# Performance work log

Hardware: AMD Instinct MI355X
Metric: run time of the kernel (lower is better)

## Reference

```python
import jax, jax.numpy as jnp
import numpy as np

B, N, DIM = 2, 2048, 1024
HEADS, DIM_HEAD = 16, 64
INNER = HEADS * DIM_HEAD  # 1024
SCALE = DIM_HEAD ** -0.5


def setup_inputs() -> dict:
    key = jax.random.key(0)
    ks = jax.random.split(key, 6)
    s = lambda k, shape, fan: jax.random.normal(k, shape, jnp.float32) * (fan ** -0.5)
    return {
        "x": jax.random.normal(ks[0], (B, N, DIM), jnp.float32),
        "similarity": jax.random.normal(ks[1], (B, N), jnp.float32),
        "Wq": s(ks[2], (DIM, INNER), DIM),
        "Wkv": s(ks[3], (DIM, 2 * INNER), DIM),
        "Wo": s(ks[4], (INNER, DIM), INNER),
        "bo": jnp.zeros((DIM,), jnp.float32),
    }


def reference(x, similarity, Wq, Wkv, Wo, bo):
    b, n, _ = x.shape
    h, d = HEADS, DIM_HEAD
    # projections (context = x, self-attention)
    q = (x @ Wq).reshape(b, n, h, d).transpose(0, 2, 1, 3)        # b h n d
    kv = x @ Wkv                                                   # b n 2*inner
    k, v = jnp.split(kv, 2, axis=-1)
    k = k.reshape(b, n, h, d).transpose(0, 2, 1, 3)
    v = v.reshape(b, n, h, d).transpose(0, 2, 1, 3)
    dots = jnp.einsum('bhid,bhjd->bhij', q, k) * SCALE             # b h n n
    # similarity [b,n] -> broadcast as per-query row bias [b,1,n,1]
    dots = dots + similarity[:, None, :, None]
    attn = jax.nn.softmax(dots, axis=-1)
    out = jnp.einsum('bhij,bhjd->bhid', attn, v)                   # b h n d
    out = out.transpose(0, 2, 1, 3).reshape(b, n, h * d)           # b n inner
    return out @ Wo + bo
```

## Files before the change

### kernel.cpp

```cpp
#include <hip/hip_runtime.h>


typedef __attribute__((ext_vector_type(8))) short short8;
typedef __attribute__((ext_vector_type(4))) float float4_;
typedef __attribute__((ext_vector_type(4))) unsigned short ushort4_;

#define MFMA(a, b, c) __builtin_amdgcn_mfma_f32_16x16x32_bf16((a), (b), (c), 0, 0, 0)

static __device__ __forceinline__ unsigned short f2bf(float f) {
    union { float f; unsigned int u; } v; v.f = f;
    unsigned int r = v.u + 0x7FFFu + ((v.u >> 16) & 1u);
    return (unsigned short)(r >> 16);
}

static __device__ __forceinline__ void gld16(const void* g, void* l) {
    __builtin_amdgcn_global_load_lds(
        (__attribute__((address_space(1))) void*)(g),
        (__attribute__((address_space(3))) void*)(l), 16, 0, 0);
}

__global__ __launch_bounds__(256) void prep(
    const float* __restrict__ X, const float* __restrict__ Wq,
    const float* __restrict__ Wkv, const float* __restrict__ Wo,
    unsigned short* __restrict__ xb, unsigned short* __restrict__ Wt,
    unsigned short* __restrict__ Wot)
{
    const int bid = blockIdx.x, t = threadIdx.x;
    if (bid >= 1024) {
        const int b = bid - 1024;
        const float4_* src = (const float4_*)X;
        ushort4_* dst = (ushort4_*)xb;
        #pragma unroll
        for (int g = 0; g < 8; ++g) {
            const int idx = b * 2048 + g * 256 + t;
            float4_ v = src[idx];
            ushort4_ o;
            o[0] = f2bf(v[0]); o[1] = f2bf(v[1]);
            o[2] = f2bf(v[2]); o[3] = f2bf(v[3]);
            dst[idx] = o;
        }
        return;
    }
    __shared__ float tile[64][65];
    const float* src; unsigned short* dst; int N, kt, nt, drow0;
    if (bid < 256)      { src = Wq;  N = 1024; kt = bid & 15;       nt = bid >> 4;       dst = Wt;  drow0 = nt * 64; }
    else if (bid < 768) { src = Wkv; N = 2048; kt = (bid-256) & 15; nt = (bid-256) >> 4; dst = Wt;  drow0 = 1024 + nt * 64; }
    else                { src = Wo;  N = 1024; kt = (bid-768) & 15; nt = (bid-768) >> 4; dst = Wot; drow0 = nt * 64; }
    const int k0 = kt * 64, n0 = nt * 64;
    const int r0 = t >> 6, c = t & 63;
    #pragma unroll
    for (int i = 0; i < 16; ++i) {
        const int r = i * 4 + r0;
        tile[r][c] = src[(size_t)(k0 + r) * N + n0 + c];
    }
    __syncthreads();
    #pragma unroll
    for (int i = 0; i < 16; ++i) {
        const int rn = i * 4 + r0;
        dst[(size_t)(drow0 + rn) * 1024 + k0 + c] = f2bf(tile[c][rn]);
    }
}

__global__ __launch_bounds__(256) void qkv_gemm2(
    const unsigned short* __restrict__ xb, const unsigned short* __restrict__ Wt,
    unsigned short* __restrict__ q_ws, unsigned short* __restrict__ k_ws,
    unsigned short* __restrict__ vt_ws)
{
    __shared__ unsigned short As[128 * 64];
    __shared__ unsigned short Bs[128 * 64];
    const int t = threadIdx.x, wave = t >> 6, lane = t & 63;
    const int L = lane & 15, quad = lane >> 4;
    const int mb = blockIdx.x / 24, nb = blockIdx.x % 24;
    const int m0 = mb * 128, n0 = nb * 128;
    const int wr = wave >> 1, wc = wave & 1;

    float4_ z = {0.f, 0.f, 0.f, 0.f};
    float4_ acc[4][4];
    #pragma unroll
    for (int i = 0; i < 4; ++i)
        #pragma unroll
        for (int j = 0; j < 4; ++j) acc[i][j] = z;

    const unsigned short* gA[4]; const unsigned short* gB[4];
    unsigned short* lA[4]; unsigned short* lB[4];
    #pragma unroll
    for (int j = 0; j < 4; ++j) {
        const int cid = wave * 256 + j * 64 + lane;
        const int row = cid >> 3, pc = cid & 7;
        const int lch = pc ^ (row & 7);
        gA[j] = xb + (size_t)(m0 + row) * 1024 + lch * 8;
        gB[j] = Wt + (size_t)(n0 + row) * 1024 + lch * 8;
        lA[j] = As + wave * 2048 + j * 512;
        lB[j] = Bs + wave * 2048 + j * 512;
    }

    for (int kc = 0; kc < 1024; kc += 64) {
        #pragma unroll
        for (int j = 0; j < 4; ++j) {
            gld16(gA[j] + kc, lA[j]);
            gld16(gB[j] + kc, lB[j]);
        }
        __syncthreads();
        #pragma unroll
        for (int ks = 0; ks < 2; ++ks) {
            short8 af[4], bfr[4];
            #pragma unroll
            for (int mt = 0; mt < 4; ++mt) {
                const int rl = wr * 64 + mt * 16 + L;
                af[mt] = *(const short8*)(As + rl * 64 + (((ks * 4 + quad) ^ (L & 7)) << 3));
            }
            #pragma unroll
            for (int nt = 0; nt < 4; ++nt) {
                const int rl = wc * 64 + nt * 16 + L;
                bfr[nt] = *(const short8*)(Bs + rl * 64 + (((ks * 4 + quad) ^ (L & 7)) << 3));
            }
            #pragma unroll
            for (int mt = 0; mt < 4; ++mt)
                #pragma unroll
                for (int nt = 0; nt < 4; ++nt)
                    acc[mt][nt] = MFMA(af[mt], bfr[nt], acc[mt][nt]);
        }
        __syncthreads();
    }

    const int b = m0 >> 11;
    const int type = n0 >> 10;
    #pragma unroll
    for (int mt = 0; mt < 4; ++mt) {
        const int m = (m0 & 2047) + wr * 64 + mt * 16 + quad * 4;
        #pragma unroll
        for (int nt = 0; nt < 4; ++nt) {
            const int cl = (n0 & 1023) + wc * 64 + nt * 16 + L;
            const int h = cl >> 6, d = cl & 63;
            float4_ v = acc[mt][nt];
            if (type == 0) {
                unsigned short* p = q_ws + ((size_t)(b * 16 + h) * 2048 + m) * 64 + d;
                #pragma unroll
                for (int r = 0; r < 4; ++r) p[(size_t)r * 64] = f2bf(v[r] * 0.18033688011f);
            } else if (type == 1) {
                unsigned short* p = k_ws + ((size_t)(b * 16 + h) * 2048 + m) * 64 + d;
                #pragma unroll
                for (int r = 0; r < 4; ++r) p[(size_t)r * 64] = f2bf(v[r]);
            } else {
                ushort4_ pk;
                pk[0] = f2bf(v[0]); pk[1] = f2bf(v[1]);
                pk[2] = f2bf(v[2]); pk[3] = f2bf(v[3]);
                *(ushort4_*)(vt_ws + ((size_t)(b * 16 + h) * 64 + d) * 2048 + m) = pk;
            }
        }
    }
}

__global__ __launch_bounds__(256) void attn_fwd(
    const unsigned short* __restrict__ q_ws,
    const unsigned short* __restrict__ k_ws,
    const unsigned short* __restrict__ vt_ws,
    unsigned short* __restrict__ o2)
{
    __shared__ unsigned short k_lds[64][72];
    __shared__ unsigned short v_lds[64][72];
    __shared__ unsigned short p_lds[64][72];
    const int t = threadIdx.x, wave = t >> 6, lane = t & 63;
    const int L = lane & 15, quad = lane >> 4;
    const int bh = blockIdx.x >> 5, qb = blockIdx.x & 31;

    const unsigned short* Kp = k_ws + (size_t)bh * 2048 * 64;
    const unsigned short* Vt = vt_ws + (size_t)bh * 64 * 2048;
    const unsigned short* Qp = q_ws + ((size_t)bh * 2048 + qb * 64 + wave * 16 + L) * 64;
    short8 qf0 = *(const short8*)(Qp + quad * 8);
    short8 qf1 = *(const short8*)(Qp + 32 + quad * 8);

    float4_ z = {0.f, 0.f, 0.f, 0.f};
    float lsum[4] = {0.f, 0.f, 0.f, 0.f};
    float4_ o[4];
    #pragma unroll
    for (int dt = 0; dt < 4; ++dt) o[dt] = z;

    const int sr = t >> 2, sc = (t & 3) * 16;
    const unsigned short* kg_base = Kp + (size_t)sr * 64 + sc;
    const unsigned short* vg_base = Vt + (size_t)sr * 2048 + sc;

    for (int j0 = 0; j0 < 2048; j0 += 64) {
        __syncthreads();
        short8 kv0 = *(const short8*)(kg_base + (size_t)j0 * 64);
        short8 kv1 = *(const short8*)(kg_base + (size_t)j0 * 64 + 8);
        short8 vv0 = *(const short8*)(vg_base + j0);
        short8 vv1 = *(const short8*)(vg_base + j0 + 8);
        *(short8*)&k_lds[sr][sc]     = kv0;
        *(short8*)&k_lds[sr][sc + 8] = kv1;
        *(short8*)&v_lds[sr][sc]     = vv0;
        *(short8*)&v_lds[sr][sc + 8] = vv1;
        __syncthreads();

        float4_ s[4];
        #pragma unroll
        for (int nt = 0; nt < 4; ++nt) s[nt] = z;
        #pragma unroll
        for (int nt = 0; nt < 4; ++nt) {
            short8 b0 = *(const short8*)&k_lds[nt * 16 + L][quad * 8];
            short8 b1 = *(const short8*)&k_lds[nt * 16 + L][32 + quad * 8];
            s[nt] = MFMA(qf0, b0, s[nt]);
            s[nt] = MFMA(qf1, b1, s[nt]);
        }

        #pragma unroll
        for (int nt = 0; nt < 4; ++nt)
            #pragma unroll
            for (int r = 0; r < 4; ++r) {
                float p = __builtin_amdgcn_exp2f(s[nt][r]);
                s[nt][r] = p;
                lsum[r] += p;
            }

        #pragma unroll
        for (int nt = 0; nt < 4; ++nt)
            #pragma unroll
            for (int r = 0; r < 4; ++r) {
                union { float f; unsigned int u; } cv; cv.f = s[nt][r];
                p_lds[wave * 16 + quad * 4 + r][nt * 16 + L] = (unsigned short)(cv.u >> 16);
            }

        #pragma unroll
        for (int ks = 0; ks < 2; ++ks) {
            short8 pa = *(const short8*)&p_lds[wave * 16 + L][ks * 32 + quad * 8];
            #pragma unroll
            for (int dt = 0; dt < 4; ++dt) {
                short8 vb = *(const short8*)&v_lds[dt * 16 + L][ks * 32 + quad * 8];
                o[dt] = MFMA(pa, vb, o[dt]);
            }
        }
    }

    float inv[4];
    #pragma unroll
    for (int r = 0; r < 4; ++r) {
        float l = lsum[r];
        l += __shfl_xor(l, 1); l += __shfl_xor(l, 2);
        l += __shfl_xor(l, 4); l += __shfl_xor(l, 8);
        inv[r] = 1.0f / l;
    }
    const int b = bh >> 4, h = bh & 15;
    unsigned short* op = o2 + ((size_t)b * 2048 + qb * 64 + wave * 16 + quad * 4) * 1024 + h * 64 + L;
    #pragma unroll
    for (int dt = 0; dt < 4; ++dt)
        #pragma unroll
        for (int r = 0; r < 4; ++r)
            op[(size_t)r * 1024 + dt * 16] = f2bf(o[dt][r] * inv[r]);
}

__global__ __launch_bounds__(256) void out_gemm2(
    const unsigned short* __restrict__ o2, const unsigned short* __restrict__ Wot,
    const float* __restrict__ bo, float* __restrict__ Out)
{
    __shared__ unsigned short As[128 * 64];
    __shared__ unsigned short Bs[64 * 64];
    const int t = threadIdx.x, wave = t >> 6, lane = t & 63;
    const int L = lane & 15, quad = lane >> 4;
    const int mb = blockIdx.x >> 4, nb = blockIdx.x & 15;
    const int m0 = mb * 128, n0 = nb * 64;
    const int wr = wave >> 1, wc = wave & 1;

    float4_ z = {0.f, 0.f, 0.f, 0.f};
    float4_ acc[4][2];
    #pragma unroll
    for (int i = 0; i < 4; ++i)
        #pragma unroll
        for (int j = 0; j < 2; ++j) acc[i][j] = z;

    const unsigned short* gA[4]; unsigned short* lA[4];
    #pragma unroll
    for (int j = 0; j < 4; ++j) {
        const int cid = wave * 256 + j * 64 + lane;
        const int row = cid >> 3, pc = cid & 7;
        gA[j] = o2 + (size_t)(m0 + row) * 1024 + (pc ^ (row & 7)) * 8;
        lA[j] = As + wave * 2048 + j * 512;
    }
    const unsigned short* gB[2]; unsigned short* lB[2];
    #pragma unroll
    for (int j = 0; j < 2; ++j) {
        const int cid = wave * 128 + j * 64 + lane;
        const int row = cid >> 3, pc = cid & 7;
        gB[j] = Wot + (size_t)(n0 + row) * 1024 + (pc ^ (row & 7)) * 8;
        lB[j] = Bs + wave * 1024 + j * 512;
    }

    for (int kc = 0; kc < 1024; kc += 64) {
        #pragma unroll
        for (int j = 0; j < 4; ++j) gld16(gA[j] + kc, lA[j]);
        #pragma unroll
        for (int j = 0; j < 2; ++j) gld16(gB[j] + kc, lB[j]);
        __syncthreads();
        #pragma unroll
        for (int ks = 0; ks < 2; ++ks) {
            short8 af[4], bfr[2];
            #pragma unroll
            for (int mt = 0; mt < 4; ++mt) {
                const int rl = wr * 64 + mt * 16 + L;
                af[mt] = *(const short8*)(As + rl * 64 + (((ks * 4 + quad) ^ (L & 7)) << 3));
            }
            #pragma unroll
            for (int nt = 0; nt < 2; ++nt) {
                const int rl = wc * 32 + nt * 16 + L;
                bfr[nt] = *(const short8*)(Bs + rl * 64 + (((ks * 4 + quad) ^ (L & 7)) << 3));
            }
            #pragma unroll
            for (int mt = 0; mt < 4; ++mt)
                #pragma unroll
                for (int nt = 0; nt < 2; ++nt)
                    acc[mt][nt] = MFMA(af[mt], bfr[nt], acc[mt][nt]);
        }
        __syncthreads();
    }

    #pragma unroll
    for (int mt = 0; mt < 4; ++mt) {
        const int m = m0 + wr * 64 + mt * 16 + quad * 4;
        #pragma unroll
        for (int nt = 0; nt < 2; ++nt) {
            const int c = n0 + wc * 32 + nt * 16 + L;
            const float bias = bo[c];
            #pragma unroll
            for (int r = 0; r < 4; ++r)
                Out[(size_t)(m + r) * 1024 + c] = acc[mt][nt][r] + bias;
        }
    }
}

extern "C" void kernel_launch(void* const* d_in, const int* in_sizes, int n_in,
                              void* d_out, int out_size, void* d_ws, size_t ws_size,
                              hipStream_t stream) {
    const float* x   = (const float*)d_in[0];
    const float* Wq  = (const float*)d_in[2];
    const float* Wkv = (const float*)d_in[3];
    const float* Wo  = (const float*)d_in[4];
    const float* bo  = (const float*)d_in[5];
    float* out = (float*)d_out;

    char* ws = (char*)d_ws;
    const size_t MB = 1024 * 1024;
    unsigned short* xb   = (unsigned short*)(ws);
    unsigned short* o2   = xb;
    unsigned short* Wt   = (unsigned short*)(ws + 8 * MB);
    unsigned short* Wot  = (unsigned short*)(ws + 14 * MB);
    unsigned short* q_ws = (unsigned short*)(ws + 16 * MB);
    unsigned short* k_ws = (unsigned short*)(ws + 24 * MB);
    unsigned short* vt_ws= (unsigned short*)(ws + 32 * MB);

    prep<<<dim3(1536), dim3(256), 0, stream>>>(x, Wq, Wkv, Wo, xb, Wt, Wot);
    qkv_gemm2<<<dim3(768), dim3(256), 0, stream>>>(xb, Wt, q_ws, k_ws, vt_ws);
    attn_fwd<<<dim3(1024), dim3(256), 0, stream>>>(q_ws, k_ws, vt_ws, o2);
    out_gemm2<<<dim3(512), dim3(256), 0, stream>>>(o2, Wot, bo, out);
}
```

Before: 210.8 us.

## Rewrite attention with 32x32 MFMA, double-buffered async K/V loads, swizzled LDS

Rebuilds the attention kernel around 32x32x16 bf16 MFMA tiles, so each wave handles 32 query rows and each block 128. K and V tiles are now loaded straight into LDS with global_load_lds into two buffers, so the next tile's fetch overlaps the current tile's compute. Row padding in LDS is replaced by an XOR swizzle, and there is one barrier per iteration instead of two. This doubles per-wave work and halves the grid, trading more register pressure and fewer blocks for better MFMA efficiency and reuse of K/V across queries.

```diff
diff --git a/kernel.cpp b/kernel.cpp
--- a/kernel.cpp
+++ b/kernel.cpp
@@ -3,9 +3,11 @@
 
 typedef __attribute__((ext_vector_type(8))) short short8;
 typedef __attribute__((ext_vector_type(4))) float float4_;
+typedef __attribute__((ext_vector_type(16))) float floatx16;
 typedef __attribute__((ext_vector_type(4))) unsigned short ushort4_;
 
 #define MFMA(a, b, c) __builtin_amdgcn_mfma_f32_16x16x32_bf16((a), (b), (c), 0, 0, 0)
+#define MFMA32(a, b, c) __builtin_amdgcn_mfma_f32_32x32x16_bf16((a), (b), (c), 0, 0, 0)
 
 static __device__ __forceinline__ unsigned short f2bf(float f) {
     union { float f; unsigned int u; } v; v.f = f;
@@ -151,101 +153,117 @@
     }
 }
 
-__global__ __launch_bounds__(256) void attn_fwd(
+__global__ __launch_bounds__(256) void attn_fwd2(
     const unsigned short* __restrict__ q_ws,
     const unsigned short* __restrict__ k_ws,
     const unsigned short* __restrict__ vt_ws,
     unsigned short* __restrict__ o2)
 {
-    __shared__ unsigned short k_lds[64][72];
-    __shared__ unsigned short v_lds[64][72];
-    __shared__ unsigned short p_lds[64][72];
+    __shared__ unsigned short k_lds[2][64 * 64];
+    __shared__ unsigned short v_lds[2][64 * 64];
+    __shared__ unsigned short p_lds[128 * 64];
     const int t = threadIdx.x, wave = t >> 6, lane = t & 63;
-    const int L = lane & 15, quad = lane >> 4;
-    const int bh = blockIdx.x >> 5, qb = blockIdx.x & 31;
+    const int l32 = lane & 31, hi = lane >> 5;
+    const int bh = blockIdx.x >> 4, qb = blockIdx.x & 15;
 
     const unsigned short* Kp = k_ws + (size_t)bh * 2048 * 64;
     const unsigned short* Vt = vt_ws + (size_t)bh * 64 * 2048;
-    const unsigned short* Qp = q_ws + ((size_t)bh * 2048 + qb * 64 + wave * 16 + L) * 64;
-    short8 qf0 = *(const short8*)(Qp + quad * 8);
-    short8 qf1 = *(const short8*)(Qp + 32 + quad * 8);
-
-    float4_ z = {0.f, 0.f, 0.f, 0.f};
-    float lsum[4] = {0.f, 0.f, 0.f, 0.f};
-    float4_ o[4];
-    #pragma unroll
-    for (int dt = 0; dt < 4; ++dt) o[dt] = z;
-
-    const int sr = t >> 2, sc = (t & 3) * 16;
-    const unsigned short* kg_base = Kp + (size_t)sr * 64 + sc;
-    const unsigned short* vg_base = Vt + (size_t)sr * 2048 + sc;
+
+    const unsigned short* Qp = q_ws + ((size_t)bh * 2048 + qb * 128 + wave * 32 + l32) * 64;
+    short8 qf[4];
+    #pragma unroll
+    for (int s = 0; s < 4; ++s) qf[s] = *(const short8*)(Qp + hi * 8 + s * 16);
+
+    const int c0 = wave * 64 + lane;
+    const int kr0 = c0 >> 3, kl0 = (c0 & 7) ^ (kr0 & 7);
+    const int kr1 = kr0 + 32, kl1 = kl0;
+    const unsigned short* ks0 = Kp + (size_t)kr0 * 64 + kl0 * 8;
+    const unsigned short* ks1 = Kp + (size_t)kr1 * 64 + kl1 * 8;
+    const unsigned short* vs0 = Vt + (size_t)kr0 * 2048 + kl0 * 8;
+    const unsigned short* vs1 = Vt + (size_t)kr1 * 2048 + kl1 * 8;
+    const int dst0 = wave * 512, dst1 = 2048 + wave * 512;
+
+    floatx16 o0 = {0.f}, o1 = {0.f};
+    #pragma unroll
+    for (int r = 0; r < 16; ++r) { o0[r] = 0.f; o1[r] = 0.f; }
+    float lsum[16];
+    #pragma unroll
+    for (int r = 0; r < 16; ++r) lsum[r] = 0.f;
+
+    gld16(ks0, k_lds[0] + dst0); gld16(ks1, k_lds[0] + dst1);
+    gld16(vs0, v_lds[0] + dst0); gld16(vs1, v_lds[0] + dst1);
+    __syncthreads();
+
+    const int prow = wave * 32 + l32;
+    const int myrow[4] = {0, 1, 2, 3};
 
     for (int j0 = 0; j0 < 2048; j0 += 64) {
-        __syncthreads();
-        short8 kv0 = *(const short8*)(kg_base + (size_t)j0 * 64);
-        short8 kv1 = *(const short8*)(kg_base + (size_t)j0 * 64 + 8);
-        short8 vv0 = *(const short8*)(vg_base + j0);
-        short8 vv1 = *(const short8*)(vg_base + j0 + 8);
-        *(short8*)&k_lds[sr][sc]     = kv0;
-        *(short8*)&k_lds[sr][sc + 8] = kv1;
-        *(short8*)&v_lds[sr][sc]     = vv0;
-        *(short8*)&v_lds[sr][sc + 8] = vv1;
-        __syncthreads();
-
-        float4_ s[4];
-        #pragma unroll
-        for (int nt = 0; nt < 4; ++nt) s[nt] = z;
-        #pragma unroll
-        for (int nt = 0; nt < 4; ++nt) {
-            short8 b0 = *(const short8*)&k_lds[nt * 16 + L][quad * 8];
-            short8 b1 = *(const short8*)&k_lds[nt * 16 + L][32 + quad * 8];
-            s[nt] = MFMA(qf0, b0, s[nt]);
-            s[nt] = MFMA(qf1, b1, s[nt]);
-        }
-
-        #pragma unroll
-        for (int nt = 0; nt < 4; ++nt)
-            #pragma unroll
-            for (int r = 0; r < 4; ++r) {
-                float p = __builtin_amdgcn_exp2f(s[nt][r]);
-                s[nt][r] = p;
-                lsum[r] += p;
-            }
-
-        #pragma unroll
-        for (int nt = 0; nt < 4; ++nt)
-            #pragma unroll
-            for (int r = 0; r < 4; ++r) {
-                union { float f; unsigned int u; } cv; cv.f = s[nt][r];
-                p_lds[wave * 16 + quad * 4 + r][nt * 16 + L] = (unsigned short)(cv.u >> 16);
-            }
-
-        #pragma unroll
-        for (int ks = 0; ks < 2; ++ks) {
-            short8 pa = *(const short8*)&p_lds[wave * 16 + L][ks * 32 + quad * 8];
-            #pragma unroll
-            for (int dt = 0; dt < 4; ++dt) {
-                short8 vb = *(const short8*)&v_lds[dt * 16 + L][ks * 32 + quad * 8];
-                o[dt] = MFMA(pa, vb, o[dt]);
-            }
-        }
-    }
-
-    float inv[4];
-    #pragma unroll
-    for (int r = 0; r < 4; ++r) {
+        const int p = (j0 >> 6) & 1;
+        if (j0 + 64 < 2048) {
+            const int np = p ^ 1;
+            gld16(ks0 + (j0 + 64) * 64, k_lds[np] + dst0);
+            gld16(ks1 + (j0 + 64) * 64, k_lds[np] + dst1);
+            gld16(vs0 + (j0 + 64), v_lds[np] + dst0);
+            gld16(vs1 + (j0 + 64), v_lds[np] + dst1);
+        }
+        const unsigned short* kb = k_lds[p];
+        const unsigned short* vb = v_lds[p];
+
+        floatx16 s0 = o0, s1 = o0;
+        #pragma unroll
+        for (int r = 0; r < 16; ++r) { s0[r] = 0.f; s1[r] = 0.f; }
+        #pragma unroll
+        for (int s = 0; s < 4; ++s) {
+            const int lch = hi + 2 * s;
+            short8 k0 = *(const short8*)(kb + l32 * 64 + ((lch ^ (l32 & 7)) << 3));
+            short8 k1 = *(const short8*)(kb + (32 + l32) * 64 + ((lch ^ (l32 & 7)) << 3));
+            s0 = MFMA32(qf[s], k0, s0);
+            s1 = MFMA32(qf[s], k1, s1);
+        }
+
+        #pragma unroll
+        for (int r = 0; r < 16; ++r) {
+            const int row = wave * 32 + (r & 3) + 8 * (r >> 2) + 4 * hi;
+            float p0 = __builtin_amdgcn_exp2f(s0[r]);
+            float p1 = __builtin_amdgcn_exp2f(s1[r]);
+            lsum[r] += p0 + p1;
+            union { float f; unsigned int u; } cv0, cv1;
+            cv0.f = p0; cv1.f = p1;
+            const int ch0 = (l32 >> 3) ^ (row & 7);
+            const int ch1 = (4 + (l32 >> 3)) ^ (row & 7);
+            p_lds[row * 64 + ch0 * 8 + (l32 & 7)] = (unsigned short)(cv0.u >> 16);
+            p_lds[row * 64 + ch1 * 8 + (l32 & 7)] = (unsigned short)(cv1.u >> 16);
+        }
+
+        #pragma unroll
+        for (int s = 0; s < 4; ++s) {
+            const int lch = hi + 2 * s;
+            short8 pa = *(const short8*)(p_lds + prow * 64 + ((lch ^ (prow & 7)) << 3));
+            short8 v0 = *(const short8*)(vb + l32 * 64 + ((lch ^ (l32 & 7)) << 3));
+            short8 v1 = *(const short8*)(vb + (32 + l32) * 64 + ((lch ^ (l32 & 7)) << 3));
+            o0 = MFMA32(pa, v0, o0);
+            o1 = MFMA32(pa, v1, o1);
+        }
+        __syncthreads();
+    }
+
+    float inv[16];
+    #pragma unroll
+    for (int r = 0; r < 16; ++r) {
         float l = lsum[r];
         l += __shfl_xor(l, 1); l += __shfl_xor(l, 2);
         l += __shfl_xor(l, 4); l += __shfl_xor(l, 8);
+        l += __shfl_xor(l, 16);
         inv[r] = 1.0f / l;
     }
     const int b = bh >> 4, h = bh & 15;
-    unsigned short* op = o2 + ((size_t)b * 2048 + qb * 64 + wave * 16 + quad * 4) * 1024 + h * 64 + L;
-    #pragma unroll
-    for (int dt = 0; dt < 4; ++dt)
-        #pragma unroll
-        for (int r = 0; r < 4; ++r)
-            op[(size_t)r * 1024 + dt * 16] = f2bf(o[dt][r] * inv[r]);
+    unsigned short* ob = o2 + ((size_t)b * 2048 + qb * 128 + wave * 32) * 1024 + h * 64;
+    #pragma unroll
+    for (int r = 0; r < 16; ++r) {
+        const int row = (r & 3) + 8 * (r >> 2) + 4 * hi;
+        ob[(size_t)row * 1024 + l32]      = f2bf(o0[r] * inv[r]);
+        ob[(size_t)row * 1024 + 32 + l32] = f2bf(o1[r] * inv[r]);
+    }
 }
 
 __global__ __launch_bounds__(256) void out_gemm2(
@@ -348,6 +366,6 @@
 
     prep<<<dim3(1536), dim3(256), 0, stream>>>(x, Wq, Wkv, Wo, xb, Wt, Wot);
     qkv_gemm2<<<dim3(768), dim3(256), 0, stream>>>(xb, Wt, q_ws, k_ws, vt_ws);
-    attn_fwd<<<dim3(1024), dim3(256), 0, stream>>>(q_ws, k_ws, vt_ws, o2);
+    attn_fwd2<<<dim3(512), dim3(256), 0, stream>>>(q_ws, k_ws, vt_ws, o2);
     out_gemm2<<<dim3(512), dim3(256), 0, stream>>>(o2, Wot, bo, out);
 }
```

Result: no change. 208.2 us (-1.2%).
